# Kernel optimization log

Hardware: AMD Instinct MI355X
Metric: run time of the kernel (lower is better)

## Reference

```python
import jax, jax.numpy as jnp
import numpy as np

N_FEAT = 32
EPS = 1e-7


def _normalize_gate(g1, g2, g3):
    s = jnp.abs(g1) + jnp.abs(g2) + jnp.abs(g3) + EPS
    m = (s >= 1.0).astype(g1.dtype)
    norm = lambda g: (1.0 - m) * g + m * (g / s)
    return norm(g1), norm(g2), norm(g3)


def _gate_recurrent(xm, g1, g2, g3, horizontal, reverse):
    """SPN GateRecurrent2dnoind. xm,g*: [B,C,H,W].
    h(t) = (1-g1-g2-g3)*x(t) + g1*h_prev(k-1) + g2*h_prev(k) + g3*h_prev(k+1),
    scanned over W (horizontal) or H (vertical); out-of-range h := 0.
    """
    if horizontal:
        perm, inv = (3, 0, 1, 2), (1, 2, 3, 0)   # [W,B,C,H], cross dim = H
    else:
        perm, inv = (2, 0, 1, 3), (1, 2, 0, 3)   # [H,B,C,W], cross dim = W
    xt = jnp.transpose(xm, perm)
    a = jnp.transpose(g1, perm)
    b = jnp.transpose(g2, perm)
    c = jnp.transpose(g3, perm)

    def step(h, inp):
        x_t, a_t, b_t, c_t = inp
        zero = jnp.zeros_like(h[..., :1])
        h_m = jnp.concatenate([zero, h[..., :-1]], axis=-1)  # h_prev(k-1)
        h_p = jnp.concatenate([h[..., 1:], zero], axis=-1)   # h_prev(k+1)
        h_new = (1.0 - a_t - b_t - c_t) * x_t + a_t * h_m + b_t * h + c_t * h_p
        return h_new, h_new

    init = jnp.zeros_like(xt[0])
    _, ys = jax.lax.scan(step, init, (xt, a, b, c), reverse=reverse)
    return jnp.transpose(ys, inv)


def setup_inputs() -> dict:
    key = jax.random.key(0)
    k1, k2 = jax.random.split(key)
    x = jax.random.normal(k1, (4, 12 * N_FEAT, 256, 256), dtype=jnp.float32)
    mask = jax.random.normal(k2, (4, N_FEAT, 256, 256), dtype=jnp.float32)
    return {"x": x, "mask": mask}


def reference(x, mask):
    nf = N_FEAT
    gs = [x[:, k * nf:(k + 1) * nf] for k in range(12)]
    outs = []
    dirs = [(True, False), (True, True), (False, False), (False, True)]
    for d, (horiz, rev) in enumerate(dirs):
        g1, g2, g3 = _normalize_gate(gs[3 * d], gs[3 * d + 1], gs[3 * d + 2])
        outs.append(_gate_recurrent(mask, g1, g2, g3, horiz, rev))
    return jnp.maximum(jnp.maximum(outs[0], outs[1]), jnp.maximum(outs[2], outs[3]))
```

## Files before the change

### kernel.cpp

```cpp
#include <hip/hip_runtime.h>

#define HW 256
#define NF 32
#define TCOLS 8

__device__ __forceinline__ unsigned enc(float f) {
  unsigned u = __float_as_uint(f);
  return u ^ (0x80000000u | (unsigned)((int)u >> 31));
}
__device__ __forceinline__ float dec(unsigned k) {
  unsigned b = (k & 0x80000000u) ? (k ^ 0x80000000u) : ~k;
  return __uint_as_float(b);
}

__device__ __forceinline__ float stepf(float a, float b, float c, float xm,
                                       float hm, float hc, float hp) {
  float s = fabsf(a) + fabsf(b) + fabsf(c) + 1e-7f;
  float inv = __builtin_amdgcn_rcpf(s);
  if (s < 1.0f) inv = 1.0f;
  a *= inv; b *= inv; c *= inv;
  float h = (1.0f - a - b - c) * xm;
  h = fmaf(a, hm, h);
  h = fmaf(b, hc, h);
  h = fmaf(c, hp, h);
  return h;
}

__global__ __launch_bounds__(256) void spn_scan_ws(
    const float* __restrict__ x, const float* __restrict__ mask,
    float* __restrict__ ws) {
  const int bid = blockIdx.x;
  const int tid = threadIdx.x;
  const size_t plane = (size_t)HW * HW;
  const size_t P = (size_t)4 * NF * plane;

  if (bid < 256) {
    __shared__ float tl[4][TCOLS][HW];
    __shared__ float hb[2][HW + 2];
    const int dir = bid >> 7;
    const int rem = bid & 127;
    const int b = rem >> 5, ch = rem & 31;
    const bool rev = (dir == 1);
    const float* g1p = x + ((size_t)b * 12 * NF + (3 * dir + 0) * NF + ch) * plane;
    const float* g2p = x + ((size_t)b * 12 * NF + (3 * dir + 1) * NF + ch) * plane;
    const float* g3p = x + ((size_t)b * 12 * NF + (3 * dir + 2) * NF + ch) * plane;
    const float* mp  = mask + ((size_t)b * NF + ch) * plane;
    float* wdir = ws + (size_t)dir * P + ((size_t)b * NF + ch) * plane;

    for (int i = tid; i < 2 * (HW + 2); i += 256) (&hb[0][0])[i] = 0.0f;

    float hreg = 0.0f;
    int cur = 0;
    float res[TCOLS], prev[TCOLS];
    int pt0 = 0;
    const int r0 = tid >> 1, cc = tid & 1;
    const float* ps[4] = {g1p, g2p, g3p, mp};
    for (int tile = 0; tile < HW / TCOLS; ++tile) {
      const int t0 = rev ? (HW - TCOLS - tile * TCOLS) : (tile * TCOLS);
      __syncthreads();
      if (tile > 0) {
        float4 v0 = {prev[0], prev[1], prev[2], prev[3]};
        float4 v1 = {prev[4], prev[5], prev[6], prev[7]};
        *(float4*)(wdir + (size_t)tid * HW + pt0) = v0;
        *(float4*)(wdir + (size_t)tid * HW + pt0 + 4) = v1;
      }
#pragma unroll
      for (int p = 0; p < 4; ++p) {
#pragma unroll
        for (int half = 0; half < 2; ++half) {
          const int r = r0 + half * 128;
          const float4 v = *(const float4*)(ps[p] + (size_t)r * HW + t0 + cc * 4);
          tl[p][cc * 4 + 0][r] = v.x;
          tl[p][cc * 4 + 1][r] = v.y;
          tl[p][cc * 4 + 2][r] = v.z;
          tl[p][cc * 4 + 3][r] = v.w;
        }
      }
      __syncthreads();
#pragma unroll
      for (int j = 0; j < TCOLS; ++j) {
        const int col = rev ? (TCOLS - 1 - j) : j;
        const float a  = tl[0][col][tid];
        const float g2 = tl[1][col][tid];
        const float c  = tl[2][col][tid];
        const float xm = tl[3][col][tid];
        const float hm = hb[cur][tid];
        const float hp = hb[cur][tid + 2];
        const float h = stepf(a, g2, c, xm, hm, hreg, hp);
        hb[cur ^ 1][tid + 1] = h;
        hreg = h;
        res[col] = h;
        __syncthreads();
        cur ^= 1;
      }
#pragma unroll
      for (int k = 0; k < TCOLS; ++k) prev[k] = res[k];
      pt0 = t0;
    }
    {
      float4 v0 = {prev[0], prev[1], prev[2], prev[3]};
      float4 v1 = {prev[4], prev[5], prev[6], prev[7]};
      *(float4*)(wdir + (size_t)tid * HW + pt0) = v0;
      *(float4*)(wdir + (size_t)tid * HW + pt0 + 4) = v1;
    }
  } else {
    const int lane = tid & 63;
    const int sid = (bid - 256) * 4 + (tid >> 6);
    const int dir = 2 + (sid >> 7);
    const int rem = sid & 127;
    const int b = rem >> 5, ch = rem & 31;
    const bool rev = (dir == 3);
    const float* g1p = x + ((size_t)b * 12 * NF + (3 * dir + 0) * NF + ch) * plane;
    const float* g2p = x + ((size_t)b * 12 * NF + (3 * dir + 1) * NF + ch) * plane;
    const float* g3p = x + ((size_t)b * 12 * NF + (3 * dir + 2) * NF + ch) * plane;
    const float* mp  = mask + ((size_t)b * NF + ch) * plane;
    float* wdir = ws + (size_t)dir * P + ((size_t)b * NF + ch) * plane;

    const int koff = lane * 4;
    float4 hv = {0.f, 0.f, 0.f, 0.f};
    float4 Ab[4], Bb[4], Cb[4], Xb[4];
#pragma unroll
    for (int p = 0; p < 4; ++p) {
      const int t = rev ? (HW - 1 - p) : p;
      const size_t ro = (size_t)t * HW + koff;
      Ab[p] = *(const float4*)(g1p + ro);
      Bb[p] = *(const float4*)(g2p + ro);
      Cb[p] = *(const float4*)(g3p + ro);
      Xb[p] = *(const float4*)(mp + ro);
    }

#define VSTEP(s, ph)                                                        \
  {                                                                         \
    const int t = rev ? (HW - 1 - (s)) : (s);                               \
    const float4 A = Ab[ph], Bv = Bb[ph], Cv = Cb[ph], X = Xb[ph];          \
    float left = __shfl_up(hv.w, 1);                                        \
    if (lane == 0) left = 0.f;                                              \
    float right = __shfl_down(hv.x, 1);                                     \
    if (lane == 63) right = 0.f;                                            \
    float4 hn;                                                              \
    hn.x = stepf(A.x, Bv.x, Cv.x, X.x, left, hv.x, hv.y);                   \
    hn.y = stepf(A.y, Bv.y, Cv.y, X.y, hv.x, hv.y, hv.z);                   \
    hn.z = stepf(A.z, Bv.z, Cv.z, X.z, hv.y, hv.z, hv.w);                   \
    hn.w = stepf(A.w, Bv.w, Cv.w, X.w, hv.z, hv.w, right);                  \
    *(float4*)(wdir + (size_t)t * HW + koff) = hn;                          \
    const int sn = (s) + 4;                                                 \
    if (sn < HW) {                                                          \
      const int tn = rev ? (HW - 1 - sn) : sn;                              \
      const size_t ro = (size_t)tn * HW + koff;                             \
      Ab[ph] = *(const float4*)(g1p + ro);                                  \
      Bb[ph] = *(const float4*)(g2p + ro);                                  \
      Cb[ph] = *(const float4*)(g3p + ro);                                  \
      Xb[ph] = *(const float4*)(mp + ro);                                   \
    }                                                                       \
    hv = hn;                                                                \
  }

    for (int s = 0; s < HW; s += 4) {
      VSTEP(s + 0, 0);
      VSTEP(s + 1, 1);
      VSTEP(s + 2, 2);
      VSTEP(s + 3, 3);
    }
#undef VSTEP
  }
}

__global__ __launch_bounds__(256) void spn_combine(
    const float4* __restrict__ w0, const float4* __restrict__ w1,
    const float4* __restrict__ w2, const float4* __restrict__ w3,
    float4* __restrict__ o) {
  const int i = blockIdx.x * 256 + threadIdx.x;
  const float4 a = w0[i], b = w1[i], c = w2[i], d = w3[i];
  float4 r;
  r.x = fmaxf(fmaxf(a.x, b.x), fmaxf(c.x, d.x));
  r.y = fmaxf(fmaxf(a.y, b.y), fmaxf(c.y, d.y));
  r.z = fmaxf(fmaxf(a.z, b.z), fmaxf(c.z, d.z));
  r.w = fmaxf(fmaxf(a.w, b.w), fmaxf(c.w, d.w));
  o[i] = r;
}

__global__ __launch_bounds__(256) void spn_scan_atomic(
    const float* __restrict__ x, const float* __restrict__ mask,
    unsigned* __restrict__ out) {
  const int bid = blockIdx.x;
  const int tid = threadIdx.x;
  __shared__ float tl[4][TCOLS][HW];
  __shared__ float hb[2][HW + 2];
  const size_t plane = (size_t)HW * HW;

  if (bid < 256) {
    const int dir = bid >> 7;
    const int rem = bid & 127;
    const int b = rem >> 5, ch = rem & 31;
    const bool rev = (dir == 1);
    const float* g1p = x + ((size_t)b * 12 * NF + (3 * dir + 0) * NF + ch) * plane;
    const float* g2p = x + ((size_t)b * 12 * NF + (3 * dir + 1) * NF + ch) * plane;
    const float* g3p = x + ((size_t)b * 12 * NF + (3 * dir + 2) * NF + ch) * plane;
    const float* mp  = mask + ((size_t)b * NF + ch) * plane;
    unsigned* op = out + ((size_t)b * NF + ch) * plane;

    for (int i = tid; i < 2 * (HW + 2); i += 256) (&hb[0][0])[i] = 0.0f;

    float hreg = 0.0f;
    int cur = 0;
    const int r0 = tid >> 1, cc = tid & 1;
    const float* ps[4] = {g1p, g2p, g3p, mp};
    for (int tile = 0; tile < HW / TCOLS; ++tile) {
      const int t0 = rev ? (HW - TCOLS - tile * TCOLS) : (tile * TCOLS);
      __syncthreads();
#pragma unroll
      for (int p = 0; p < 4; ++p) {
#pragma unroll
        for (int half = 0; half < 2; ++half) {
          const int r = r0 + half * 128;
          const float4 v = *(const float4*)(ps[p] + (size_t)r * HW + t0 + cc * 4);
          tl[p][cc * 4 + 0][r] = v.x;
          tl[p][cc * 4 + 1][r] = v.y;
          tl[p][cc * 4 + 2][r] = v.z;
          tl[p][cc * 4 + 3][r] = v.w;
        }
      }
      __syncthreads();
      for (int j = 0; j < TCOLS; ++j) {
        const int col = rev ? (TCOLS - 1 - j) : j;
        const int t = t0 + col;
        const float a  = tl[0][col][tid];
        const float g2 = tl[1][col][tid];
        const float c  = tl[2][col][tid];
        const float xm = tl[3][col][tid];
        const float hm = hb[cur][tid];
        const float hp = hb[cur][tid + 2];
        const float h = stepf(a, g2, c, xm, hm, hreg, hp);
        hb[cur ^ 1][tid + 1] = h;
        hreg = h;
        atomicMax(op + (size_t)tid * HW + t, enc(h));
        __syncthreads();
        cur ^= 1;
      }
    }
  } else {
    if (tid >= 64) return;
    const int lane = tid;
    const int vb = bid - 256;
    const int dir = 2 + (vb >> 7);
    const int rem = vb & 127;
    const int b = rem >> 5, ch = rem & 31;
    const bool rev = (dir == 3);
    const float* g1p = x + ((size_t)b * 12 * NF + (3 * dir + 0) * NF + ch) * plane;
    const float* g2p = x + ((size_t)b * 12 * NF + (3 * dir + 1) * NF + ch) * plane;
    const float* g3p = x + ((size_t)b * 12 * NF + (3 * dir + 2) * NF + ch) * plane;
    const float* mp  = mask + ((size_t)b * NF + ch) * plane;
    unsigned* op = out + ((size_t)b * NF + ch) * plane;

    float4 hv = {0.f, 0.f, 0.f, 0.f};
    int t = rev ? (HW - 1) : 0;
    const int koff = lane * 4;
    float4 a4 = *(const float4*)(g1p + (size_t)t * HW + koff);
    float4 b4 = *(const float4*)(g2p + (size_t)t * HW + koff);
    float4 c4 = *(const float4*)(g3p + (size_t)t * HW + koff);
    float4 x4 = *(const float4*)(mp  + (size_t)t * HW + koff);
    for (int step = 0; step < HW; ++step) {
      const float4 A = a4, B = b4, C = c4, X = x4;
      const int tn = rev ? (HW - 2 - step) : (step + 1);
      if (step + 1 < HW) {
        a4 = *(const float4*)(g1p + (size_t)tn * HW + koff);
        b4 = *(const float4*)(g2p + (size_t)tn * HW + koff);
        c4 = *(const float4*)(g3p + (size_t)tn * HW + koff);
        x4 = *(const float4*)(mp  + (size_t)tn * HW + koff);
      }
      float left = __shfl_up(hv.w, 1);
      if (lane == 0) left = 0.f;
      float right = __shfl_down(hv.x, 1);
      if (lane == 63) right = 0.f;
      float4 hn;
      hn.x = stepf(A.x, B.x, C.x, X.x, left, hv.x, hv.y);
      hn.y = stepf(A.y, B.y, C.y, X.y, hv.x, hv.y, hv.z);
      hn.z = stepf(A.z, B.z, C.z, X.z, hv.y, hv.z, hv.w);
      hn.w = stepf(A.w, B.w, C.w, X.w, hv.z, hv.w, right);
      unsigned* o = op + (size_t)t * HW + koff;
      atomicMax(o + 0, enc(hn.x));
      atomicMax(o + 1, enc(hn.y));
      atomicMax(o + 2, enc(hn.z));
      atomicMax(o + 3, enc(hn.w));
      hv = hn;
      t = tn;
    }
  }
}

__global__ __launch_bounds__(256) void spn_decode(unsigned* __restrict__ o) {
  const int i = blockIdx.x * 256 + threadIdx.x;
  uint4 v = ((uint4*)o)[i];
  float4 f;
  f.x = dec(v.x); f.y = dec(v.y); f.z = dec(v.z); f.w = dec(v.w);
  ((float4*)o)[i] = f;
}

extern "C" void kernel_launch(void* const* d_in, const int* in_sizes, int n_in,
                              void* d_out, int out_size, void* d_ws, size_t ws_size,
                              hipStream_t stream) {
  const float* x = (const float*)d_in[0];
  const float* mask = (const float*)d_in[1];
  (void)in_sizes; (void)n_in;
  const size_t need = (size_t)4 * out_size * sizeof(float);
  if (ws_size >= need) {
    float* ws = (float*)d_ws;
    spn_scan_ws<<<320, 256, 0, stream>>>(x, mask, ws);
    const size_t P4 = (size_t)out_size / 4;
    spn_combine<<<out_size / 1024, 256, 0, stream>>>(
        (const float4*)ws, (const float4*)(ws + (size_t)out_size),
        (const float4*)(ws + 2 * (size_t)out_size),
        (const float4*)(ws + 3 * (size_t)out_size), (float4*)d_out);
    (void)P4;
  } else {
    hipMemsetAsync(d_out, 0, (size_t)out_size * sizeof(float), stream);
    spn_scan_atomic<<<512, 256, 0, stream>>>(x, mask, (unsigned*)d_out);
    spn_decode<<<out_size / 1024, 256, 0, stream>>>((unsigned*)d_out);
  }
}
```

Baseline: 757.6 us.

## Use single-wave blocks for horizontal scans with shuffle neighbors and register prefetch

The horizontal-direction scans now run one 64-lane wavefront per (direction, batch, channel), each lane owning four adjacent rows. Neighbor hidden states move through lane shuffles instead of a shared-memory buffer with a block barrier on every column step. The next 8-column tile of gates and mask is prefetched into 32 float4 registers while the current tile is computed, and results are written back as float4 per row. In exchange, register pressure rises sharply, the grid grows to 512 single-wave blocks, and only a single wave is left to hide load latency during the LDS transpose.

```diff
diff --git a/kernel.cpp b/kernel.cpp
--- a/kernel.cpp
+++ b/kernel.cpp
@@ -11,6 +11,10 @@
 __device__ __forceinline__ float dec(unsigned k) {
   unsigned b = (k & 0x80000000u) ? (k ^ 0x80000000u) : ~k;
   return __uint_as_float(b);
+}
+
+__device__ __forceinline__ float4 mk4(float a, float b, float c, float d) {
+  float4 v; v.x = a; v.y = b; v.z = c; v.w = d; return v;
 }
 
 __device__ __forceinline__ float stepf(float a, float b, float c, float xm,
@@ -26,17 +30,36 @@
   return h;
 }
 
-__global__ __launch_bounds__(256) void spn_scan_ws(
+
+#define COL_STEP(jj)                                                        \
+  {                                                                         \
+    const float4 A  = *(const float4*)&tl[0][jj][4 * lane];                 \
+    const float4 Bv = *(const float4*)&tl[1][jj][4 * lane];                 \
+    const float4 Cv = *(const float4*)&tl[2][jj][4 * lane];                 \
+    const float4 X  = *(const float4*)&tl[3][jj][4 * lane];                 \
+    float left = __shfl_up(hv.w, 1);                                        \
+    if (lane == 0) left = 0.f;                                              \
+    float right = __shfl_down(hv.x, 1);                                     \
+    if (lane == 63) right = 0.f;                                            \
+    float4 hn;                                                              \
+    hn.x = stepf(A.x, Bv.x, Cv.x, X.x, left, hv.x, hv.y);                   \
+    hn.y = stepf(A.y, Bv.y, Cv.y, X.y, hv.x, hv.y, hv.z);                   \
+    hn.z = stepf(A.z, Bv.z, Cv.z, X.z, hv.y, hv.z, hv.w);                   \
+    hn.w = stepf(A.w, Bv.w, Cv.w, X.w, hv.z, hv.w, right);                  \
+    res[jj] = hn;                                                           \
+    hv = hn;                                                                \
+  }
+
+__global__ __launch_bounds__(64, 1) void spn_scan_ws(
     const float* __restrict__ x, const float* __restrict__ mask,
     float* __restrict__ ws) {
   const int bid = blockIdx.x;
-  const int tid = threadIdx.x;
+  const int lane = threadIdx.x;
   const size_t plane = (size_t)HW * HW;
-  const size_t P = (size_t)4 * NF * plane;
+  const size_t PBUF = (size_t)4 * NF * plane;
 
   if (bid < 256) {
     __shared__ float tl[4][TCOLS][HW];
-    __shared__ float hb[2][HW + 2];
     const int dir = bid >> 7;
     const int rem = bid & 127;
     const int b = rem >> 5, ch = rem & 31;
@@ -45,67 +68,63 @@
     const float* g2p = x + ((size_t)b * 12 * NF + (3 * dir + 1) * NF + ch) * plane;
     const float* g3p = x + ((size_t)b * 12 * NF + (3 * dir + 2) * NF + ch) * plane;
     const float* mp  = mask + ((size_t)b * NF + ch) * plane;
-    float* wdir = ws + (size_t)dir * P + ((size_t)b * NF + ch) * plane;
-
-    for (int i = tid; i < 2 * (HW + 2); i += 256) (&hb[0][0])[i] = 0.0f;
-
-    float hreg = 0.0f;
-    int cur = 0;
-    float res[TCOLS], prev[TCOLS];
-    int pt0 = 0;
-    const int r0 = tid >> 1, cc = tid & 1;
+    float* wdir = ws + (size_t)dir * PBUF + ((size_t)b * NF + ch) * plane;
     const float* ps[4] = {g1p, g2p, g3p, mp};
-    for (int tile = 0; tile < HW / TCOLS; ++tile) {
-      const int t0 = rev ? (HW - TCOLS - tile * TCOLS) : (tile * TCOLS);
-      __syncthreads();
-      if (tile > 0) {
-        float4 v0 = {prev[0], prev[1], prev[2], prev[3]};
-        float4 v1 = {prev[4], prev[5], prev[6], prev[7]};
-        *(float4*)(wdir + (size_t)tid * HW + pt0) = v0;
-        *(float4*)(wdir + (size_t)tid * HW + pt0 + 4) = v1;
-      }
-#pragma unroll
-      for (int p = 0; p < 4; ++p) {
-#pragma unroll
-        for (int half = 0; half < 2; ++half) {
-          const int r = r0 + half * 128;
-          const float4 v = *(const float4*)(ps[p] + (size_t)r * HW + t0 + cc * 4);
-          tl[p][cc * 4 + 0][r] = v.x;
-          tl[p][cc * 4 + 1][r] = v.y;
-          tl[p][cc * 4 + 2][r] = v.z;
-          tl[p][cc * 4 + 3][r] = v.w;
+
+    const int r_lo = lane >> 1;
+    const int c0 = (lane & 1) * 4;
+    float4 Pr[32];
+    float4 hv = mk4(0.f, 0.f, 0.f, 0.f);
+
+    int t0 = rev ? (HW - TCOLS) : 0;
+#pragma unroll
+    for (int q = 0; q < 32; ++q) {
+      const int p = q >> 3, pass = q & 7;
+      Pr[q] = *(const float4*)(ps[p] + (size_t)(pass * 32 + r_lo) * HW + t0 + c0);
+    }
+
+    for (int k = 0; k < HW / TCOLS; ++k) {
+#pragma unroll
+      for (int q = 0; q < 32; ++q) {
+        const int p = q >> 3, pass = q & 7;
+        const int r = pass * 32 + r_lo;
+        tl[p][c0 + 0][r] = Pr[q].x;
+        tl[p][c0 + 1][r] = Pr[q].y;
+        tl[p][c0 + 2][r] = Pr[q].z;
+        tl[p][c0 + 3][r] = Pr[q].w;
+      }
+      const int t0c = t0;
+      t0 += rev ? -TCOLS : TCOLS;
+      if (k + 1 < HW / TCOLS) {
+#pragma unroll
+        for (int q = 0; q < 32; ++q) {
+          const int p = q >> 3, pass = q & 7;
+          Pr[q] = *(const float4*)(ps[p] + (size_t)(pass * 32 + r_lo) * HW + t0 + c0);
         }
       }
-      __syncthreads();
-#pragma unroll
-      for (int j = 0; j < TCOLS; ++j) {
-        const int col = rev ? (TCOLS - 1 - j) : j;
-        const float a  = tl[0][col][tid];
-        const float g2 = tl[1][col][tid];
-        const float c  = tl[2][col][tid];
-        const float xm = tl[3][col][tid];
-        const float hm = hb[cur][tid];
-        const float hp = hb[cur][tid + 2];
-        const float h = stepf(a, g2, c, xm, hm, hreg, hp);
-        hb[cur ^ 1][tid + 1] = h;
-        hreg = h;
-        res[col] = h;
-        __syncthreads();
-        cur ^= 1;
-      }
-#pragma unroll
-      for (int k = 0; k < TCOLS; ++k) prev[k] = res[k];
-      pt0 = t0;
-    }
-    {
-      float4 v0 = {prev[0], prev[1], prev[2], prev[3]};
-      float4 v1 = {prev[4], prev[5], prev[6], prev[7]};
-      *(float4*)(wdir + (size_t)tid * HW + pt0) = v0;
-      *(float4*)(wdir + (size_t)tid * HW + pt0 + 4) = v1;
+      asm volatile("s_waitcnt lgkmcnt(0)" ::: "memory");
+
+      float4 res[TCOLS];
+      if (!rev) {
+        COL_STEP(0) COL_STEP(1) COL_STEP(2) COL_STEP(3)
+        COL_STEP(4) COL_STEP(5) COL_STEP(6) COL_STEP(7)
+      } else {
+        COL_STEP(7) COL_STEP(6) COL_STEP(5) COL_STEP(4)
+        COL_STEP(3) COL_STEP(2) COL_STEP(1) COL_STEP(0)
+      }
+
+      float* wr = wdir + (size_t)(4 * lane) * HW + t0c;
+      *(float4*)(wr)              = mk4(res[0].x, res[1].x, res[2].x, res[3].x);
+      *(float4*)(wr + 4)          = mk4(res[4].x, res[5].x, res[6].x, res[7].x);
+      *(float4*)(wr + HW)         = mk4(res[0].y, res[1].y, res[2].y, res[3].y);
+      *(float4*)(wr + HW + 4)     = mk4(res[4].y, res[5].y, res[6].y, res[7].y);
+      *(float4*)(wr + 2 * HW)     = mk4(res[0].z, res[1].z, res[2].z, res[3].z);
+      *(float4*)(wr + 2 * HW + 4) = mk4(res[4].z, res[5].z, res[6].z, res[7].z);
+      *(float4*)(wr + 3 * HW)     = mk4(res[0].w, res[1].w, res[2].w, res[3].w);
+      *(float4*)(wr + 3 * HW + 4) = mk4(res[4].w, res[5].w, res[6].w, res[7].w);
     }
   } else {
-    const int lane = tid & 63;
-    const int sid = (bid - 256) * 4 + (tid >> 6);
+    const int sid = bid - 256;
     const int dir = 2 + (sid >> 7);
     const int rem = sid & 127;
     const int b = rem >> 5, ch = rem & 31;
@@ -114,10 +133,10 @@
     const float* g2p = x + ((size_t)b * 12 * NF + (3 * dir + 1) * NF + ch) * plane;
     const float* g3p = x + ((size_t)b * 12 * NF + (3 * dir + 2) * NF + ch) * plane;
     const float* mp  = mask + ((size_t)b * NF + ch) * plane;
-    float* wdir = ws + (size_t)dir * P + ((size_t)b * NF + ch) * plane;
+    float* wdir = ws + (size_t)dir * PBUF + ((size_t)b * NF + ch) * plane;
 
     const int koff = lane * 4;
-    float4 hv = {0.f, 0.f, 0.f, 0.f};
+    float4 hv = mk4(0.f, 0.f, 0.f, 0.f);
     float4 Ab[4], Bb[4], Cb[4], Xb[4];
 #pragma unroll
     for (int p = 0; p < 4; ++p) {
@@ -305,13 +324,11 @@
   const size_t need = (size_t)4 * out_size * sizeof(float);
   if (ws_size >= need) {
     float* ws = (float*)d_ws;
-    spn_scan_ws<<<320, 256, 0, stream>>>(x, mask, ws);
-    const size_t P4 = (size_t)out_size / 4;
+    spn_scan_ws<<<512, 64, 0, stream>>>(x, mask, ws);
     spn_combine<<<out_size / 1024, 256, 0, stream>>>(
         (const float4*)ws, (const float4*)(ws + (size_t)out_size),
         (const float4*)(ws + 2 * (size_t)out_size),
         (const float4*)(ws + 3 * (size_t)out_size), (float4*)d_out);
-    (void)P4;
   } else {
     hipMemsetAsync(d_out, 0, (size_t)out_size * sizeof(float), stream);
     spn_scan_atomic<<<512, 256, 0, stream>>>(x, mask, (unsigned*)d_out);
```

After: 750.5 us. Within noise of the previous version (-0.9%).
